# Kernel optimization log

Measured on AMD Instinct MI355X. Metric: run time of the kernel, lower is better.

Reference implementation:

```python
import jax, jax.numpy as jnp
import numpy as np

DK = 64
DROPOUT_P = 0.1


def setup_inputs() -> dict:
    key = jax.random.key(0)
    kq, kk, kv, km = jax.random.split(key, 4)
    B, S, D = 16, 2048, 64
    q = jax.random.normal(kq, (B, S, D), dtype=jnp.float32)
    k = jax.random.normal(kk, (B, S, D), dtype=jnp.float32)
    v = jax.random.normal(kv, (B, S, D), dtype=jnp.float32)
    attn_mask = jax.random.randint(km, (S, S), 0, 2, dtype=jnp.int32)
    return {"q": q, "k": k, "v": v, "attn_mask": attn_mask}


def reference(q, k, v, attn_mask):
    # q = q / sqrt(dk)
    qs = q * (1.0 / np.sqrt(DK)).astype(np.float32)
    # dots: [B, S_q, S_k]
    dots = jnp.einsum("bqd,bkd->bqk", qs, k)
    # mask: 0 -> -inf, 1 -> 0 (additive)
    add_mask = jnp.where(attn_mask == 0, -jnp.inf, 0.0).astype(dots.dtype)
    dots = dots + add_mask  # broadcast [S,S] over batch
    attn = jax.nn.softmax(dots, axis=-1)
    # inverted dropout, train mode, fixed key for determinism
    keep = jax.random.bernoulli(jax.random.key(42), 1.0 - DROPOUT_P, attn.shape)
    attn = jnp.where(keep, attn * (1.0 / (1.0 - DROPOUT_P)), 0.0)
    out = jnp.einsum("bqk,bkd->bqd", attn, v)
    return out
```

## Files before the change

### kernel.cpp

```cpp
#include <hip/hip_runtime.h>

#define BATCH 16
#define SEQ   2048
#define DIM   64
#define NTHREADS 256

typedef short bf16x8 __attribute__((ext_vector_type(8)));
typedef float f32x4 __attribute__((ext_vector_type(4)));

__device__ __forceinline__ int ldsoff(int row) {
  return row * 72 + 16 * (row >> 2);
}
#define LDS_SZ (64 * 72 + 16 * 16)

__device__ __forceinline__ unsigned tf_bits(unsigned f) {
  unsigned x0 = 0u;
  unsigned x1 = f;
  const unsigned ks1 = 42u;
  const unsigned ks2 = 0x1BD11BDAu ^ 42u;
  x1 += ks1;
#define TF_R(r) { x0 += x1; x1 = __builtin_amdgcn_alignbit(x1, x1, 32u - (r)); x1 ^= x0; }
  TF_R(13) TF_R(15) TF_R(26) TF_R(6)
  x0 += ks1; x1 += ks2 + 1u;
  TF_R(17) TF_R(29) TF_R(16) TF_R(24)
  x0 += ks2; x1 += 2u;
  TF_R(13) TF_R(15) TF_R(26) TF_R(6)
  x1 += ks1 + 3u;
  TF_R(17) TF_R(29) TF_R(16) TF_R(24)
  x0 += ks1; x1 += ks2 + 4u;
  TF_R(13) TF_R(15) TF_R(26) TF_R(6)
  x0 += ks2; x1 += 5u;
#undef TF_R
  return x0 ^ x1;
}
#define KEEP_THRESH 0xE6666600u

__device__ __forceinline__ unsigned pack_bf16x2(float lo, float hi) {
  const unsigned l = (__float_as_uint(lo) + 0x8000u) >> 16;
  const unsigned h = (__float_as_uint(hi) + 0x8000u) & 0xFFFF0000u;
  return h | l;
}
__device__ __forceinline__ unsigned pack_trunc(float lo, float hi) {
  return __builtin_amdgcn_perm(__float_as_uint(hi), __float_as_uint(lo), 0x07060302u);
}

#define WS_KF 0
#define WS_VF 1048576
#define WS_MB 2097152
#define WS_O0 2228224
#define WS_O1 4325376
#define WS_L  6422528

__global__ __launch_bounds__(NTHREADS)
void prep(const float* __restrict__ k, const float* __restrict__ v,
          const int* __restrict__ mask, unsigned* __restrict__ ws) {
  const int t = threadIdx.x;
  const unsigned bx = blockIdx.x;

  if (bx < 2048) {
    const int x = (int)bx & 7;
    const int j = (int)bx >> 3;
    const int b = 2 * x + (j & 1);
    const int inner = j >> 1;
    const int kv = inner >> 6;
    const int idx = inner & 63;
    const unsigned e = (unsigned)b * 16384u + (unsigned)idx * 256u + (unsigned)t;
    const int lane = t & 63;
    const int tx = lane & 15, quad = lane >> 4;
    const int ks = (e >> 6) & 1, nt = (e >> 7) & 3, kt = (e >> 9) & 31;
    uint4 wout;
    if (kv == 0) {
      const float* src = k + ((size_t)b * SEQ + kt * 64 + 4 * tx + nt) * DIM
                           + ks * 32 + quad * 8;
      const float4 f0 = *(const float4*)src;
      const float4 f1 = *(const float4*)(src + 4);
      wout.x = pack_bf16x2(f0.x, f0.y); wout.y = pack_bf16x2(f0.z, f0.w);
      wout.z = pack_bf16x2(f1.x, f1.y); wout.w = pack_bf16x2(f1.z, f1.w);
      *(uint4*)(ws + WS_KF + (size_t)e * 4) = wout;
    } else {
      const float* src = v + ((size_t)b * SEQ + kt * 64 + ks * 32 + quad * 8) * DIM
                           + nt * 16 + tx;
      const float a0 = src[0 * DIM], a1 = src[1 * DIM], a2 = src[2 * DIM], a3 = src[3 * DIM];
      const float a4 = src[4 * DIM], a5 = src[5 * DIM], a6 = src[6 * DIM], a7 = src[7 * DIM];
      wout.x = pack_bf16x2(a0, a1); wout.y = pack_bf16x2(a2, a3);
      wout.z = pack_bf16x2(a4, a5); wout.w = pack_bf16x2(a6, a7);
      *(uint4*)(ws + WS_VF + (size_t)e * 4) = wout;
    }
    return;
  }

  const unsigned pid = (bx - 2048u) * NTHREADS + (unsigned)t;
  const unsigned C4 = pid & 511u, R4 = pid >> 9;
  unsigned m16 = 0u;
#pragma unroll
  for (int rr = 0; rr < 4; ++rr) {
    const int4 mv = *(const int4*)(mask + (size_t)(4 * R4 + rr) * SEQ + 4 * C4);
    m16 |= (mv.x ? 1u : 0u) << (rr * 4 + 0);
    m16 |= (mv.y ? 1u : 0u) << (rr * 4 + 1);
    m16 |= (mv.z ? 1u : 0u) << (rr * 4 + 2);
    m16 |= (mv.w ? 1u : 0u) << (rr * 4 + 3);
  }
  ((unsigned short*)(ws + WS_MB))[pid] = (unsigned short)m16;
}

__global__ __launch_bounds__(NTHREADS, 6)
void attn_fwd(const float* __restrict__ q, const unsigned* __restrict__ ws,
              float* __restrict__ out) {
  __shared__ unsigned short PS[LDS_SZ];

  const int t    = threadIdx.x;
  const int w    = t >> 6;
  const int lane = t & 63;
  const int tx   = lane & 15;
  const int quad = lane >> 4;

  const int x  = (int)blockIdx.x & 7;
  const int j  = (int)blockIdx.x >> 3;
  const int bb = 2 * x + (j & 1);
  const int j2 = j >> 1;
  const int q0 = (j2 & 31) * 64;
  const int sk = j2 >> 5;
  const int qw = q0 + 16 * w;
  const int kt0 = sk * 11;
  const int ktend = (sk == 2) ? 32 : kt0 + 11;

  const float qscale = 0.125f * 1.44269504088896340736f;

  bf16x8 aq[2];
  {
    const float* qr = q + ((size_t)bb * SEQ + qw + tx) * DIM + quad * 8;
#pragma unroll
    for (int ks = 0; ks < 2; ++ks) {
      const float4 f0 = *(const float4*)(qr + ks * 32);
      const float4 f1 = *(const float4*)(qr + ks * 32 + 4);
      union { unsigned u[4]; bf16x8 v; } a;
      a.u[0] = pack_bf16x2(f0.x * qscale, f0.y * qscale);
      a.u[1] = pack_bf16x2(f0.z * qscale, f0.w * qscale);
      a.u[2] = pack_bf16x2(f1.x * qscale, f1.y * qscale);
      a.u[3] = pack_bf16x2(f1.z * qscale, f1.w * qscale);
      aq[ks] = a.v;
    }
  }

  float lrun[4] = {0.f, 0.f, 0.f, 0.f};
  f32x4 oacc[4];
#pragma unroll
  for (int nt = 0; nt < 4; ++nt) oacc[nt] = (f32x4){0.f, 0.f, 0.f, 0.f};

  const unsigned* kfb = ws + WS_KF + (size_t)(bb * 32) * 2048 + (size_t)lane * 4;
  const unsigned* vfb = ws + WS_VF + (size_t)(bb * 32) * 2048 + (size_t)lane * 4;
  const unsigned short* maskp = (const unsigned short*)(ws + WS_MB)
      + ((size_t)((qw >> 2) + quad)) * 512 + tx;
  const unsigned fbase0 = (unsigned)(bb * SEQ + qw + quad * 4) * (unsigned)SEQ
                          + (unsigned)(4 * tx);

  bf16x8 vf[4][2];

#define RNG_PWRITE(kt_, qk_, mw_)                                              \
  {                                                                            \
    const unsigned fb = fbase0 + (unsigned)((kt_) * 64);                       \
    _Pragma("unroll")                                                          \
    for (int reg = 0; reg < 4; ++reg) {                                        \
      const unsigned mnib = (mw_) >> (reg * 4);                                \
      float pd[4];                                                             \
      float ls = 0.0f;                                                         \
      _Pragma("unroll")                                                        \
      for (int nt = 0; nt < 4; ++nt) {                                         \
        const float s = (mnib & (1u << nt)) ? qk_[nt][reg] : -1e30f;           \
        const float e = __builtin_amdgcn_exp2f(s);                             \
        ls += e;                                                               \
        const unsigned bits = tf_bits(fb + (unsigned)(reg * SEQ) + (unsigned)nt); \
        pd[nt] = (bits < KEEP_THRESH) ? e : 0.0f;                              \
      }                                                                        \
      lrun[reg] += ls;                                                         \
      uint2 pw;                                                                \
      pw.x = pack_trunc(pd[0], pd[1]);                                         \
      pw.y = pack_trunc(pd[2], pd[3]);                                         \
      *(uint2*)&PS[ldsoff(16 * w + quad * 4 + reg) + 4 * tx] = pw;             \
    }                                                                          \
  }

#define LOAD_KF(kt_)                                                           \
    const unsigned* kfp = kfb + (size_t)(kt_) * 2048;                          \
    bf16x8 kf[4][2];                                                           \
    _Pragma("unroll")                                                          \
    for (int nt = 0; nt < 4; ++nt)                                             \
      _Pragma("unroll")                                                        \
      for (int ks = 0; ks < 2; ++ks)                                           \
        kf[nt][ks] = *(const bf16x8*)(kfp + (nt * 2 + ks) * 256);

#define PV_STEP                                                                \
    _Pragma("unroll")                                                          \
    for (int ks = 0; ks < 2; ++ks) {                                           \
      const bf16x8 ap = *(const bf16x8*)&PS[ldsoff(16 * w + tx) + ks * 32 + quad * 8]; \
      _Pragma("unroll")                                                        \
      for (int nt = 0; nt < 4; ++nt)                                           \
        oacc[nt] = __builtin_amdgcn_mfma_f32_16x16x32_bf16(ap, vf[nt][ks],     \
                                                           oacc[nt], 0, 0, 0); \
    }

#define LOAD_VF(kt_)                                                           \
    const unsigned* vfp = vfb + (size_t)(kt_) * 2048;                          \
    _Pragma("unroll")                                                          \
    for (int nt = 0; nt < 4; ++nt)                                             \
      _Pragma("unroll")                                                        \
      for (int ks = 0; ks < 2; ++ks)                                           \
        vf[nt][ks] = *(const bf16x8*)(vfp + (nt * 2 + ks) * 256);

#define QK_STEP(qk_)                                                           \
    f32x4 qk_[4];                                                              \
    _Pragma("unroll")                                                          \
    for (int nt = 0; nt < 4; ++nt) {                                           \
      f32x4 c = (f32x4){0.f, 0.f, 0.f, 0.f};                                   \
      _Pragma("unroll")                                                        \
      for (int ks = 0; ks < 2; ++ks)                                           \
        c = __builtin_amdgcn_mfma_f32_16x16x32_bf16(aq[ks], kf[nt][ks], c, 0, 0, 0); \
      qk_[nt] = c;                                                             \
    }

  {
    LOAD_KF(kt0)
    LOAD_VF(kt0)
    const unsigned mwv = maskp[kt0 * 16];
    QK_STEP(qk)
    RNG_PWRITE(kt0, qk, mwv)
  }
#pragma unroll 1
  for (int kt = kt0 + 1; kt < ktend; ++kt) {
    LOAD_KF(kt)
    const unsigned mwv = maskp[kt * 16];
    PV_STEP
    LOAD_VF(kt)
    QK_STEP(qk)
    RNG_PWRITE(kt, qk, mwv)
  }
  PV_STEP

  float lsum[4];
#pragma unroll
  for (int reg = 0; reg < 4; ++reg) {
    float ls = lrun[reg];
    ls += __shfl_xor(ls, 1);
    ls += __shfl_xor(ls, 2);
    ls += __shfl_xor(ls, 4);
    ls += __shfl_xor(ls, 8);
    lsum[reg] = ls;
  }
  float* wsf = (float*)ws;
  const size_t off = ((size_t)bb * SEQ + qw) * DIM;
  float* ob = (sk == 0) ? wsf + WS_O0 + off
            : (sk == 1) ? wsf + WS_O1 + off
                        : out + off;
#pragma unroll
  for (int nt = 0; nt < 4; ++nt)
#pragma unroll
    for (int reg = 0; reg < 4; ++reg)
      ob[(size_t)(quad * 4 + reg) * DIM + nt * 16 + tx] = oacc[nt][reg];
  if (tx == 0) {
    float* lp = wsf + WS_L + sk * 32768 + bb * SEQ + qw + quad * 4;
#pragma unroll
    for (int reg = 0; reg < 4; ++reg) lp[reg] = lsum[reg];
  }
}

__global__ __launch_bounds__(NTHREADS)
void combine(float* __restrict__ out, const unsigned* __restrict__ ws) {
  const unsigned gid = blockIdx.x * NTHREADS + threadIdx.x;
  const float* wsf = (const float*)ws;
  const float4 a  = ((const float4*)out)[gid];
  const float4 b0 = ((const float4*)(wsf + WS_O0))[gid];
  const float4 b1 = ((const float4*)(wsf + WS_O1))[gid];
  const unsigned row = gid >> 4;
  const float linv = (1.0f / 0.9f) / (wsf[WS_L + row] + wsf[WS_L + 32768u + row]
                                      + wsf[WS_L + 65536u + row]);
  float4 o;
  o.x = (a.x + b0.x + b1.x) * linv;
  o.y = (a.y + b0.y + b1.y) * linv;
  o.z = (a.z + b0.z + b1.z) * linv;
  o.w = (a.w + b0.w + b1.w) * linv;
  ((float4*)out)[gid] = o;
}

extern "C" void kernel_launch(void* const* d_in, const int* in_sizes, int n_in,
                              void* d_out, int out_size, void* d_ws, size_t ws_size,
                              hipStream_t stream) {
  const float* q = (const float*)d_in[0];
  const float* k = (const float*)d_in[1];
  const float* v = (const float*)d_in[2];
  const int* mask = (const int*)d_in[3];
  float* out = (float*)d_out;
  unsigned* ws = (unsigned*)d_ws;

  hipLaunchKernelGGL(prep, dim3(3072), dim3(NTHREADS), 0, stream,
                     k, v, mask, ws);
  hipLaunchKernelGGL(attn_fwd, dim3(1536), dim3(NTHREADS), 0, stream,
                     q, ws, out);
  hipLaunchKernelGGL(combine, dim3(2048), dim3(NTHREADS), 0, stream, out, ws);
}
```

Baseline: 232.9 us.

## Use two-way key split, LDS-staged K/V bf16 prep, and hardware bf16 pack

Result: faster. 225.7 us (-3.1%).

```diff
diff --git a/kernel.cpp b/kernel.cpp
--- a/kernel.cpp
+++ b/kernel.cpp
@@ -43,53 +43,74 @@
 __device__ __forceinline__ unsigned pack_trunc(float lo, float hi) {
   return __builtin_amdgcn_perm(__float_as_uint(hi), __float_as_uint(lo), 0x07060302u);
 }
+__device__ __forceinline__ unsigned cvtpk(float lo, float hi) {
+  unsigned r;
+  asm("v_cvt_pk_bf16_f32 %0, %1, %2" : "=v"(r) : "v"(lo), "v"(hi));
+  return r;
+}
 
 #define WS_KF 0
 #define WS_VF 1048576
 #define WS_MB 2097152
 #define WS_O0 2228224
-#define WS_O1 4325376
-#define WS_L  6422528
+#define WS_L  4325376
 
 __global__ __launch_bounds__(NTHREADS)
 void prep(const float* __restrict__ k, const float* __restrict__ v,
           const int* __restrict__ mask, unsigned* __restrict__ ws) {
+  __shared__ float TS[64 * 68];
   const int t = threadIdx.x;
   const unsigned bx = blockIdx.x;
 
-  if (bx < 2048) {
-    const int x = (int)bx & 7;
-    const int j = (int)bx >> 3;
-    const int b = 2 * x + (j & 1);
-    const int inner = j >> 1;
-    const int kv = inner >> 6;
-    const int idx = inner & 63;
-    const unsigned e = (unsigned)b * 16384u + (unsigned)idx * 256u + (unsigned)t;
-    const int lane = t & 63;
-    const int tx = lane & 15, quad = lane >> 4;
-    const int ks = (e >> 6) & 1, nt = (e >> 7) & 3, kt = (e >> 9) & 31;
-    uint4 wout;
+  if (bx < 1024) {
+    const int x  = (int)bx & 7;
+    const int j  = (int)bx >> 3;
+    const int b  = 2 * x + (j & 1);
+    const int j2 = j >> 1;
+    const int kt = j2 & 31;
+    const int kv = j2 >> 5;
+    const float* src = (kv ? v : k) + ((size_t)b * SEQ + kt * 64) * DIM;
+
+#pragma unroll
+    for (int s = 0; s < 4; ++s) {
+      const int row = s * 16 + (t >> 4);
+      const int c4  = (t & 15) * 4;
+      *(float4*)&TS[row * 68 + c4] = *(const float4*)(src + (size_t)row * DIM + c4);
+    }
+    __syncthreads();
+
+    const int lane = t & 63, tx = lane & 15, quad = lane >> 4, sub = t >> 6;
     if (kv == 0) {
-      const float* src = k + ((size_t)b * SEQ + kt * 64 + 4 * tx + nt) * DIM
-                           + ks * 32 + quad * 8;
-      const float4 f0 = *(const float4*)src;
-      const float4 f1 = *(const float4*)(src + 4);
-      wout.x = pack_bf16x2(f0.x, f0.y); wout.y = pack_bf16x2(f0.z, f0.w);
-      wout.z = pack_bf16x2(f1.x, f1.y); wout.w = pack_bf16x2(f1.z, f1.w);
-      *(uint4*)(ws + WS_KF + (size_t)e * 4) = wout;
+#pragma unroll
+      for (int i = 0; i < 2; ++i) {
+        const int combo = sub * 2 + i, nt = combo >> 1, ks = combo & 1;
+        const float* rp = &TS[(4 * tx + nt) * 68 + ks * 32 + quad * 8];
+        const float4 f0 = *(const float4*)rp;
+        const float4 f1 = *(const float4*)(rp + 4);
+        uint4 wout;
+        wout.x = cvtpk(f0.x, f0.y); wout.y = cvtpk(f0.z, f0.w);
+        wout.z = cvtpk(f1.x, f1.y); wout.w = cvtpk(f1.z, f1.w);
+        const unsigned e = ((((unsigned)b * 32 + kt) * 4 + nt) * 2 + ks) * 64 + lane;
+        *(uint4*)(ws + WS_KF + (size_t)e * 4) = wout;
+      }
     } else {
-      const float* src = v + ((size_t)b * SEQ + kt * 64 + ks * 32 + quad * 8) * DIM
-                           + nt * 16 + tx;
-      const float a0 = src[0 * DIM], a1 = src[1 * DIM], a2 = src[2 * DIM], a3 = src[3 * DIM];
-      const float a4 = src[4 * DIM], a5 = src[5 * DIM], a6 = src[6 * DIM], a7 = src[7 * DIM];
-      wout.x = pack_bf16x2(a0, a1); wout.y = pack_bf16x2(a2, a3);
-      wout.z = pack_bf16x2(a4, a5); wout.w = pack_bf16x2(a6, a7);
-      *(uint4*)(ws + WS_VF + (size_t)e * 4) = wout;
+#pragma unroll
+      for (int i = 0; i < 2; ++i) {
+        const int combo = sub * 2 + i, nt = combo >> 1, ks = combo & 1;
+        const float* cp = &TS[(ks * 32 + quad * 8) * 68 + nt * 16 + tx];
+        uint4 wout;
+        wout.x = cvtpk(cp[0 * 68], cp[1 * 68]);
+        wout.y = cvtpk(cp[2 * 68], cp[3 * 68]);
+        wout.z = cvtpk(cp[4 * 68], cp[5 * 68]);
+        wout.w = cvtpk(cp[6 * 68], cp[7 * 68]);
+        const unsigned e = ((((unsigned)b * 32 + kt) * 4 + nt) * 2 + ks) * 64 + lane;
+        *(uint4*)(ws + WS_VF + (size_t)e * 4) = wout;
+      }
     }
     return;
   }
 
-  const unsigned pid = (bx - 2048u) * NTHREADS + (unsigned)t;
+  const unsigned pid = (bx - 1024u) * NTHREADS + (unsigned)t;
   const unsigned C4 = pid & 511u, R4 = pid >> 9;
   unsigned m16 = 0u;
 #pragma unroll
@@ -103,7 +124,7 @@
   ((unsigned short*)(ws + WS_MB))[pid] = (unsigned short)m16;
 }
 
-__global__ __launch_bounds__(NTHREADS, 6)
+__global__ __launch_bounds__(NTHREADS, 4)
 void attn_fwd(const float* __restrict__ q, const unsigned* __restrict__ ws,
               float* __restrict__ out) {
   __shared__ unsigned short PS[LDS_SZ];
@@ -121,8 +142,7 @@
   const int q0 = (j2 & 31) * 64;
   const int sk = j2 >> 5;
   const int qw = q0 + 16 * w;
-  const int kt0 = sk * 11;
-  const int ktend = (sk == 2) ? 32 : kt0 + 11;
+  const int kt0 = sk * 16;
 
   const float qscale = 0.125f * 1.44269504088896340736f;
 
@@ -226,7 +246,7 @@
     RNG_PWRITE(kt0, qk, mwv)
   }
 #pragma unroll 1
-  for (int kt = kt0 + 1; kt < ktend; ++kt) {
+  for (int kt = kt0 + 1; kt < kt0 + 16; ++kt) {
     LOAD_KF(kt)
     const unsigned mwv = maskp[kt * 16];
     PV_STEP
@@ -248,9 +268,7 @@
   }
   float* wsf = (float*)ws;
   const size_t off = ((size_t)bb * SEQ + qw) * DIM;
-  float* ob = (sk == 0) ? wsf + WS_O0 + off
-            : (sk == 1) ? wsf + WS_O1 + off
-                        : out + off;
+  float* ob = sk ? out + off : wsf + WS_O0 + off;
 #pragma unroll
   for (int nt = 0; nt < 4; ++nt)
 #pragma unroll
@@ -267,17 +285,15 @@
 void combine(float* __restrict__ out, const unsigned* __restrict__ ws) {
   const unsigned gid = blockIdx.x * NTHREADS + threadIdx.x;
   const float* wsf = (const float*)ws;
-  const float4 a  = ((const float4*)out)[gid];
-  const float4 b0 = ((const float4*)(wsf + WS_O0))[gid];
-  const float4 b1 = ((const float4*)(wsf + WS_O1))[gid];
+  const float4 a = ((const float4*)out)[gid];
+  const float4 b = ((const float4*)(wsf + WS_O0))[gid];
   const unsigned row = gid >> 4;
-  const float linv = (1.0f / 0.9f) / (wsf[WS_L + row] + wsf[WS_L + 32768u + row]
-                                      + wsf[WS_L + 65536u + row]);
+  const float linv = (1.0f / 0.9f) / (wsf[WS_L + row] + wsf[WS_L + 32768u + row]);
   float4 o;
-  o.x = (a.x + b0.x + b1.x) * linv;
-  o.y = (a.y + b0.y + b1.y) * linv;
-  o.z = (a.z + b0.z + b1.z) * linv;
-  o.w = (a.w + b0.w + b1.w) * linv;
+  o.x = (a.x + b.x) * linv;
+  o.y = (a.y + b.y) * linv;
+  o.z = (a.z + b.z) * linv;
+  o.w = (a.w + b.w) * linv;
   ((float4*)out)[gid] = o;
 }
 
@@ -291,9 +307,9 @@
   float* out = (float*)d_out;
   unsigned* ws = (unsigned*)d_ws;
 
-  hipLaunchKernelGGL(prep, dim3(3072), dim3(NTHREADS), 0, stream,
+  hipLaunchKernelGGL(prep, dim3(2048), dim3(NTHREADS), 0, stream,
                      k, v, mask, ws);
-  hipLaunchKernelGGL(attn_fwd, dim3(1536), dim3(NTHREADS), 0, stream,
+  hipLaunchKernelGGL(attn_fwd, dim3(1024), dim3(NTHREADS), 0, stream,
                      q, ws, out);
   hipLaunchKernelGGL(combine, dim3(2048), dim3(NTHREADS), 0, stream, out, ws);
 }
```
